# Kernel tuning notes

Hardware: AMD Instinct MI355X
Metric: run time of the kernel (lower is better)

## Reference

```python
import jax, jax.numpy as jnp
import numpy as np

N = 50000   # total nodes in batched graph
E = 400000  # directed edges
G = 512     # number of graphs in batch
F = 128     # input node feature dim
K = 4       # attention heads
H = 64      # hidden feats per head (flatten width = K*H = 256)
EPS = 1e-5  # BatchNorm eps


def _edge_softmax(e, dst, n):
    # softmax of per-edge scores over incoming edges of each dst node; e: [E, K]
    m = jax.ops.segment_max(e, dst, num_segments=n)
    ee = jnp.exp(e - m[dst])
    s = jax.ops.segment_sum(ee, dst, num_segments=n)
    return ee / s[dst]


def _gat_layer(x, W, al, ar, b, resW, src, dst, agg):
    # dgl GATConv with residual=True, LeakyReLU(0.2), bias, ReLU activation
    n = x.shape[0]
    z = (x @ W).reshape(n, K, H)                      # [N, K, H]
    el = jnp.einsum('nkh,kh->nk', z, al)              # [N, K]
    er = jnp.einsum('nkh,kh->nk', z, ar)
    e = jax.nn.leaky_relu(el[src] + er[dst], negative_slope=0.2)  # [E, K]
    a = _edge_softmax(e, dst, n)                      # [E, K]
    rst = jax.ops.segment_sum(a[:, :, None] * z[src], dst, num_segments=n)  # [N, K, H]
    res = (x @ resW).reshape(n, K, H) if resW is not None else x.reshape(n, K, H)
    rst = jax.nn.relu(rst + res + b.reshape(1, K, H))
    return rst.reshape(n, K * H) if agg == 'flatten' else rst.mean(axis=1)


def setup_inputs() -> dict:
    key = jax.random.key(0)
    ks = jax.random.split(key, 16)
    f32 = jnp.float32

    def p(k, shape):
        return jax.random.normal(k, shape, f32) * 0.1

    h = jax.random.normal(ks[0], (N, F), f32)
    src = jax.random.randint(ks[1], (E,), 0, N)
    dst = jax.random.randint(ks[2], (E,), 0, N)
    graph_ids = (jnp.arange(N) * G) // N  # sorted node->graph assignment, all segments nonempty

    return dict(
        h=h, src=src, dst=dst, graph_ids=graph_ids,
        W0=p(ks[3], (F, K * H)), al0=p(ks[4], (K, H)), ar0=p(ks[5], (K, H)),
        b0=jnp.zeros((K * H,), f32), resW0=p(ks[6], (F, K * H)),
        W1=p(ks[7], (K * H, K * H)), al1=p(ks[8], (K, H)), ar1=p(ks[9], (K, H)),
        b1=jnp.zeros((K * H,), f32),
        W2=p(ks[10], (K * H, K * H)), al2=p(ks[11], (K, H)), ar2=p(ks[12], (K, H)),
        b2=jnp.zeros((K * H,), f32),
        Wg=p(ks[13], (H, 1)), bg=jnp.zeros((1,), f32),
        Wm1=p(ks[14], (2 * H, H)), bm1=jnp.zeros((H,), f32),
        bn_g=jnp.ones((H,), f32), bn_b=jnp.zeros((H,), f32),
        bn_m=jnp.zeros((H,), f32), bn_v=jnp.ones((H,), f32),
        Wm2=p(ks[15], (H, 1)), bm2=jnp.zeros((1,), f32),
    )


def reference(h, src, dst, graph_ids, W0, al0, ar0, b0, resW0, W1, al1, ar1, b1,
              W2, al2, ar2, b2, Wg, bg, Wm1, bm1, bn_g, bn_b, bn_m, bn_v, Wm2, bm2):
    # 3 GAT layers: flatten, flatten, mean (dgllife GATPredictor default agg modes)
    x = _gat_layer(h, W0, al0, ar0, b0, resW0, src, dst, 'flatten')   # [N, 256]
    x = _gat_layer(x, W1, al1, ar1, b1, None, src, dst, 'flatten')    # [N, 256] (identity residual)
    x = _gat_layer(x, W2, al2, ar2, b2, None, src, dst, 'mean')       # [N, 64]
    # WeightedSumAndMax readout
    w = jax.nn.sigmoid(x @ Wg + bg)                                   # [N, 1]
    gs = jax.ops.segment_sum(w * x, graph_ids, num_segments=G)        # [G, 64]
    gm = jax.ops.segment_max(x, graph_ids, num_segments=G)            # [G, 64]
    gf = jnp.concatenate([gs, gm], axis=1)                            # [G, 128]
    # MLPPredictor (eval mode: dropout off, BatchNorm uses running stats)
    y = jax.nn.relu(gf @ Wm1 + bm1)
    y = (y - bn_m) / jnp.sqrt(bn_v + EPS) * bn_g + bn_b
    out = jax.nn.sigmoid(y @ Wm2 + bm2)                               # [G, 1]
    return out
```

## Files before the change

kernel.cpp:

```cpp
#include <hip/hip_runtime.h>
#include <math.h>


typedef _Float16 f16;
typedef _Float16 f16x4 __attribute__((ext_vector_type(4)));
typedef _Float16 f16x8 __attribute__((ext_vector_type(8)));
typedef float f32x16 __attribute__((ext_vector_type(16)));

__device__ __forceinline__ double wred_sumd(double v) {
#pragma unroll
  for (int m = 32; m > 0; m >>= 1) v += __shfl_xor(v, m, 64);
  return v;
}
__device__ __forceinline__ float wred_sum(float v) {
#pragma unroll
  for (int m = 32; m > 0; m >>= 1) v += __shfl_xor(v, m, 64);
  return v;
}

__global__ void k_hist(const int* __restrict__ dst, int* __restrict__ deg, int e) {
  int i = blockIdx.x * 256 + threadIdx.x;
  if (i < e) atomicAdd(&deg[dst[i]], 1);
}

__global__ void k_scan1(const int* __restrict__ deg, int* __restrict__ rowptr,
                        int* __restrict__ bsum, int n) {
  __shared__ int sh[256];
  int t = threadIdx.x;
  int base = blockIdx.x * 1024 + t * 4;
  int v0 = 0, v1 = 0, v2 = 0, v3 = 0;
  if (base + 0 < n) v0 = deg[base + 0];
  if (base + 1 < n) v1 = deg[base + 1];
  if (base + 2 < n) v2 = deg[base + 2];
  if (base + 3 < n) v3 = deg[base + 3];
  sh[t] = v0 + v1 + v2 + v3;
  __syncthreads();
  for (int off = 1; off < 256; off <<= 1) {
    int x = (t >= off) ? sh[t - off] : 0;
    __syncthreads();
    sh[t] += x;
    __syncthreads();
  }
  int excl = (t > 0) ? sh[t - 1] : 0;
  if (base + 0 < n) rowptr[base + 0] = excl;
  if (base + 1 < n) rowptr[base + 1] = excl + v0;
  if (base + 2 < n) rowptr[base + 2] = excl + v0 + v1;
  if (base + 3 < n) rowptr[base + 3] = excl + v0 + v1 + v2;
  if (t == 255) bsum[blockIdx.x] = sh[255];
}

__global__ void k_scan2(int* bsum, int nb) {
  if (threadIdx.x == 0 && blockIdx.x == 0) {
    int run = 0;
    for (int i = 0; i < nb; i++) { int v = bsum[i]; bsum[i] = run; run += v; }
  }
}

__global__ void k_scan3(int* __restrict__ rowptr, const int* __restrict__ bsum,
                        int n, int e) {
  int i = blockIdx.x * 256 + threadIdx.x;
  if (i < n) rowptr[i] += bsum[i >> 10];
  if (i == 0) rowptr[n] = e;
}

__global__ void k_scatter(const int* __restrict__ src, const int* __restrict__ dst,
                          const int* __restrict__ rowptr, int* __restrict__ cursor,
                          int* __restrict__ colsrc, int e) {
  int i = blockIdx.x * 256 + threadIdx.x;
  if (i < e) {
    int d = dst[i];
    int pos = rowptr[d] + atomicAdd(&cursor[d], 1);
    colsrc[pos] = src[i];
  }
}

__global__ __launch_bounds__(256) void k_split(const float* __restrict__ X,
                                               f16* __restrict__ X0,
                                               f16* __restrict__ X1, int n4) {
  int i = blockIdx.x * 256 + threadIdx.x;
  if (i >= n4) return;
  float4 v = *(const float4*)(X + (size_t)i * 4);
  f16x4 hi, lo;
  hi.x = (f16)v.x; lo.x = (f16)(v.x - (float)hi.x);
  hi.y = (f16)v.y; lo.y = (f16)(v.y - (float)hi.y);
  hi.z = (f16)v.z; lo.z = (f16)(v.z - (float)hi.z);
  hi.w = (f16)v.w; lo.w = (f16)(v.w - (float)hi.w);
  *(f16x4*)(X0 + (size_t)i * 4) = hi;
  *(f16x4*)(X1 + (size_t)i * 4) = lo;
}

__global__ void k_splitWT(const float* __restrict__ W, f16* __restrict__ P0,
                          f16* __restrict__ P1, int kin) {
  int c = blockIdx.x;
  for (int k = threadIdx.x; k < kin; k += blockDim.x) {
    float v = W[(size_t)k * 256 + c];
    f16 h0 = (f16)v;
    size_t off = ((size_t)(k >> 4) * 256 + c) * 16 + ((k >> 3) & 1) * 8 + (k & 7);
    P0[off] = h0;
    P1[off] = (f16)(v - (float)h0);
  }
}

template <int KIN>
__global__ __launch_bounds__(256) void k_gemm_mfma(
    const f16* __restrict__ X0, const f16* __restrict__ X1,
    const f16* __restrict__ WT0, const f16* __restrict__ WT1,
    float* __restrict__ C, int M) {
  __shared__ f16 aLDS[2][2][2][64][8];
  const int t = threadIdx.x;
  const int w = t >> 6;
  const int lane = t & 63;
  const int lo = lane & 31, g = lane >> 5;
  const int row0 = blockIdx.x * 64;

  f32x16 acc00, acc01, acc10, acc11;
#pragma unroll
  for (int i = 0; i < 16; i++) {
    acc00[i] = 0.f; acc01[i] = 0.f; acc10[i] = 0.f; acc11[i] = 0.f;
  }

  const size_t fb0 = (size_t)(w * 64 + lo) * 16 + g * 8;
  const size_t fb1 = (size_t)(w * 64 + 32 + lo) * 16 + g * 8;

  for (int k0 = 0; k0 < KIN; k0 += 32) {
    if (k0) __syncthreads();
#pragma unroll
    for (int ii = 0; ii < 2; ii++) {
      int c = t + ii * 256;
      int s = c >> 8, r = (c >> 2) & 63, hh = c & 3;
      int kh = hh >> 1, gg = hh & 1;
      int gr = row0 + r;
      if (gr > M - 1) gr = M - 1;
      const f16* Xs = s ? X1 : X0;
      *(float4*)&aLDS[s][r >> 5][kh][(gg << 5) | (r & 31)][0] =
          *(const float4*)&Xs[(size_t)gr * KIN + k0 + kh * 16 + gg * 8];
    }
    __syncthreads();
#pragma unroll
    for (int kh = 0; kh < 2; kh++) {
      const size_t base = (size_t)((k0 >> 4) + kh) * 4096;
      f16x8 a0r0 = *(const f16x8*)&aLDS[0][0][kh][lane][0];
      f16x8 a0r1 = *(const f16x8*)&aLDS[0][1][kh][lane][0];
      f16x8 a1r0 = *(const f16x8*)&aLDS[1][0][kh][lane][0];
      f16x8 a1r1 = *(const f16x8*)&aLDS[1][1][kh][lane][0];
      f16x8 b0c0 = *(const f16x8*)&WT0[base + fb0];
      f16x8 b0c1 = *(const f16x8*)&WT0[base + fb1];
      f16x8 b1c0 = *(const f16x8*)&WT1[base + fb0];
      f16x8 b1c1 = *(const f16x8*)&WT1[base + fb1];
      acc00 = __builtin_amdgcn_mfma_f32_32x32x16_f16(a0r0, b0c0, acc00, 0, 0, 0);
      acc01 = __builtin_amdgcn_mfma_f32_32x32x16_f16(a0r0, b0c1, acc01, 0, 0, 0);
      acc10 = __builtin_amdgcn_mfma_f32_32x32x16_f16(a0r1, b0c0, acc10, 0, 0, 0);
      acc11 = __builtin_amdgcn_mfma_f32_32x32x16_f16(a0r1, b0c1, acc11, 0, 0, 0);
      acc00 = __builtin_amdgcn_mfma_f32_32x32x16_f16(a0r0, b1c0, acc00, 0, 0, 0);
      acc01 = __builtin_amdgcn_mfma_f32_32x32x16_f16(a0r0, b1c1, acc01, 0, 0, 0);
      acc10 = __builtin_amdgcn_mfma_f32_32x32x16_f16(a0r1, b1c0, acc10, 0, 0, 0);
      acc11 = __builtin_amdgcn_mfma_f32_32x32x16_f16(a0r1, b1c1, acc11, 0, 0, 0);
      acc00 = __builtin_amdgcn_mfma_f32_32x32x16_f16(a1r0, b0c0, acc00, 0, 0, 0);
      acc01 = __builtin_amdgcn_mfma_f32_32x32x16_f16(a1r0, b0c1, acc01, 0, 0, 0);
      acc10 = __builtin_amdgcn_mfma_f32_32x32x16_f16(a1r1, b0c0, acc10, 0, 0, 0);
      acc11 = __builtin_amdgcn_mfma_f32_32x32x16_f16(a1r1, b0c1, acc11, 0, 0, 0);
    }
  }
  const int c0 = w * 64 + lo, c1 = w * 64 + 32 + lo;
#pragma unroll
  for (int reg = 0; reg < 16; reg++) {
    int rr = (reg & 3) + 8 * (reg >> 2) + 4 * g;
    int r0 = row0 + rr, r1 = row0 + 32 + rr;
    if (r0 < M) {
      C[(size_t)r0 * 256 + c0] = acc00[reg];
      C[(size_t)r0 * 256 + c1] = acc01[reg];
    }
    if (r1 < M) {
      C[(size_t)r1 * 256 + c0] = acc10[reg];
      C[(size_t)r1 * 256 + c1] = acc11[reg];
    }
  }
}

__global__ __launch_bounds__(256) void k_elr(const float* __restrict__ z,
                                             const float* __restrict__ al,
                                             const float* __restrict__ ar,
                                             float* __restrict__ el,
                                             float* __restrict__ er, int n) {
  int node = blockIdx.x * 4 + (threadIdx.x >> 6);
  int lane = threadIdx.x & 63;
  if (node >= n) return;
  const float* zr = z + (size_t)node * 256;
#pragma unroll
  for (int k = 0; k < 4; k++) {
    float zv = zr[k * 64 + lane];
    float pl = wred_sum(zv * al[k * 64 + lane]);
    float pr = wred_sum(zv * ar[k * 64 + lane]);
    if (lane == 0) {
      el[node * 4 + k] = pl;
      er[node * 4 + k] = pr;
    }
  }
}

__global__ __launch_bounds__(256) void k_att(const float* __restrict__ el,
                                             const float* __restrict__ er,
                                             const int* __restrict__ rowptr,
                                             const int* __restrict__ colsrc,
                                             float* __restrict__ a, int n) {
  int node = blockIdx.x * 4 + (threadIdx.x >> 6);
  int lane = threadIdx.x & 63;
  if (node >= n) return;
  int k = lane & 3, ii = lane >> 2;
  int base = rowptr[node];
  int deg = rowptr[node + 1] - base;
  if (deg == 0) return;
  float ernk = er[node * 4 + k];

  float m = -INFINITY;
  for (int i0 = 0; i0 < deg; i0 += 16) {
    int i = i0 + ii;
    if (i < deg) {
      int s = colsrc[base + i];
      float sc = el[s * 4 + k] + ernk;
      sc = (sc > 0.f) ? sc : 0.2f * sc;
      m = fmaxf(m, sc);
    }
  }
#pragma unroll
  for (int msk = 4; msk < 64; msk <<= 1) m = fmaxf(m, __shfl_xor(m, msk, 64));

  float ssum = 0.f;
  for (int i0 = 0; i0 < deg; i0 += 16) {
    int i = i0 + ii;
    if (i < deg) {
      int s = colsrc[base + i];
      float sc = el[s * 4 + k] + ernk;
      sc = (sc > 0.f) ? sc : 0.2f * sc;
      ssum += expf(sc - m);
    }
  }
#pragma unroll
  for (int msk = 4; msk < 64; msk <<= 1) ssum += __shfl_xor(ssum, msk, 64);
  float inv = 1.f / ssum;

  for (int i0 = 0; i0 < deg; i0 += 16) {
    int i = i0 + ii;
    if (i < deg) {
      int s = colsrc[base + i];
      float sc = el[s * 4 + k] + ernk;
      sc = (sc > 0.f) ? sc : 0.2f * sc;
      a[(size_t)(base + i) * 4 + k] = expf(sc - m) * inv;
    }
  }
}

template <int MEAN, int RESF16>
__global__ __launch_bounds__(256) void k_gather(
    const float* __restrict__ z, const float* __restrict__ a,
    const float* __restrict__ resf, const f16* __restrict__ R0,
    const f16* __restrict__ R1, const float* __restrict__ bias,
    const int* __restrict__ rowptr, const int* __restrict__ colsrc,
    float* __restrict__ out, f16* __restrict__ O0, f16* __restrict__ O1,
    float* __restrict__ wn, const float* __restrict__ Wg,
    const float* __restrict__ bg, int n) {
  const int t = threadIdx.x;
  const int w = t >> 6, lane = t & 63;
  int node = blockIdx.x * 4 + w;
  if (node > n - 1) node = n - 1;
  const int base = rowptr[node];
  const int deg = rowptr[node + 1] - base;
  const int k = lane >> 4;
  const char* zb = (const char*)z + lane * 16;

  float4 acc0 = {0, 0, 0, 0}, acc1 = {0, 0, 0, 0};
  float4 acc2 = {0, 0, 0, 0}, acc3 = {0, 0, 0, 0};
  int i = 0;
  for (; i + 4 <= deg; i += 4) {
    int s0 = colsrc[base + i + 0];
    int s1 = colsrc[base + i + 1];
    int s2 = colsrc[base + i + 2];
    int s3 = colsrc[base + i + 3];
    float a0 = a[(size_t)(base + i + 0) * 4 + k];
    float a1 = a[(size_t)(base + i + 1) * 4 + k];
    float a2 = a[(size_t)(base + i + 2) * 4 + k];
    float a3 = a[(size_t)(base + i + 3) * 4 + k];
    float4 z0 = *(const float4*)(zb + ((size_t)s0 << 10));
    float4 z1 = *(const float4*)(zb + ((size_t)s1 << 10));
    float4 z2 = *(const float4*)(zb + ((size_t)s2 << 10));
    float4 z3 = *(const float4*)(zb + ((size_t)s3 << 10));
    acc0.x = fmaf(a0, z0.x, acc0.x); acc0.y = fmaf(a0, z0.y, acc0.y);
    acc0.z = fmaf(a0, z0.z, acc0.z); acc0.w = fmaf(a0, z0.w, acc0.w);
    acc1.x = fmaf(a1, z1.x, acc1.x); acc1.y = fmaf(a1, z1.y, acc1.y);
    acc1.z = fmaf(a1, z1.z, acc1.z); acc1.w = fmaf(a1, z1.w, acc1.w);
    acc2.x = fmaf(a2, z2.x, acc2.x); acc2.y = fmaf(a2, z2.y, acc2.y);
    acc2.z = fmaf(a2, z2.z, acc2.z); acc2.w = fmaf(a2, z2.w, acc2.w);
    acc3.x = fmaf(a3, z3.x, acc3.x); acc3.y = fmaf(a3, z3.y, acc3.y);
    acc3.z = fmaf(a3, z3.z, acc3.z); acc3.w = fmaf(a3, z3.w, acc3.w);
  }
  for (; i < deg; i++) {
    int s = colsrc[base + i];
    float av = a[(size_t)(base + i) * 4 + k];
    float4 zv = *(const float4*)(zb + ((size_t)s << 10));
    acc0.x = fmaf(av, zv.x, acc0.x); acc0.y = fmaf(av, zv.y, acc0.y);
    acc0.z = fmaf(av, zv.z, acc0.z); acc0.w = fmaf(av, zv.w, acc0.w);
  }

  size_t o = (size_t)node * 256 + lane * 4;
  float4 rv;
  if (RESF16) {
    f16x4 rh = *(const f16x4*)(R0 + o);
    f16x4 rl = *(const f16x4*)(R1 + o);
    rv.x = (float)rh.x + (float)rl.x;
    rv.y = (float)rh.y + (float)rl.y;
    rv.z = (float)rh.z + (float)rl.z;
    rv.w = (float)rh.w + (float)rl.w;
  } else {
    rv = *(const float4*)(resf + o);
  }
  float4 bv = *(const float4*)(bias + lane * 4);
  float4 v;
  v.x = fmaxf(((acc0.x + acc1.x) + (acc2.x + acc3.x)) + rv.x + bv.x, 0.f);
  v.y = fmaxf(((acc0.y + acc1.y) + (acc2.y + acc3.y)) + rv.y + bv.y, 0.f);
  v.z = fmaxf(((acc0.z + acc1.z) + (acc2.z + acc3.z)) + rv.z + bv.z, 0.f);
  v.w = fmaxf(((acc0.w + acc1.w) + (acc2.w + acc3.w)) + rv.w + bv.w, 0.f);

  if (!MEAN) {
    f16x4 hi, lo;
    hi.x = (f16)v.x; lo.x = (f16)(v.x - (float)hi.x);
    hi.y = (f16)v.y; lo.y = (f16)(v.y - (float)hi.y);
    hi.z = (f16)v.z; lo.z = (f16)(v.z - (float)hi.z);
    hi.w = (f16)v.w; lo.w = (f16)(v.w - (float)hi.w);
    *(f16x4*)(O0 + o) = hi;
    *(f16x4*)(O1 + o) = lo;
  } else {
    __shared__ float tmp[4][256];
    *(float4*)&tmp[w][lane * 4] = v;
    __syncthreads();
    float xv = 0.25f * (tmp[w][lane] + tmp[w][lane + 64] + tmp[w][lane + 128] +
                        tmp[w][lane + 192]);
    out[(size_t)node * 64 + lane] = xv;
    double s = wred_sumd((double)xv * (double)Wg[lane]);
    if (lane == 0)
      wn[node] = (float)(1.0 / (1.0 + exp(-(s + (double)bg[0]))));
  }
}

__global__ __launch_bounds__(64) void k_readout(const float* __restrict__ x2,
                                                const float* __restrict__ wn,
                                                float* __restrict__ gf, int n,
                                                int g) {
  int gi = blockIdx.x;
  int lane = threadIdx.x;
  long long start = ((long long)gi * n + g - 1) / g;
  long long end = ((long long)(gi + 1) * n + g - 1) / g;
  double s = 0.0;
  float mx = -INFINITY;
  for (long long nd = start; nd < end; nd++) {
    float xv = x2[nd * 64 + lane];
    s += (double)wn[nd] * (double)xv;
    mx = fmaxf(mx, xv);
  }
  gf[gi * 128 + lane] = (float)s;
  gf[gi * 128 + 64 + lane] = mx;
}

__global__ __launch_bounds__(64) void k_mlp(const float* __restrict__ gf,
                                            const float* __restrict__ Wm1,
                                            const float* __restrict__ bm1,
                                            const float* __restrict__ bng,
                                            const float* __restrict__ bnb,
                                            const float* __restrict__ bnm,
                                            const float* __restrict__ bnv,
                                            const float* __restrict__ Wm2,
                                            const float* __restrict__ bm2,
                                            float* __restrict__ out) {
  int gi = blockIdx.x;
  int h = threadIdx.x;
  double y = (double)bm1[h];
  for (int i = 0; i < 128; i++)
    y += (double)gf[gi * 128 + i] * (double)Wm1[i * 64 + h];
  y = (y > 0.0) ? y : 0.0;
  y = (y - (double)bnm[h]) / sqrt((double)bnv[h] + 1e-5) * (double)bng[h] +
      (double)bnb[h];
  double v = wred_sumd(y * (double)Wm2[h]);
  if (h == 0) {
    double s = v + (double)bm2[0];
    out[gi] = (float)(1.0 / (1.0 + exp(-s)));
  }
}

extern "C" void kernel_launch(void* const* d_in, const int* in_sizes, int n_in,
                              void* d_out, int out_size, void* d_ws,
                              size_t ws_size, hipStream_t stream) {
  const float* h    = (const float*)d_in[0];
  const int*   src  = (const int*)d_in[1];
  const int*   dst  = (const int*)d_in[2];
  const float* W0    = (const float*)d_in[4];
  const float* al0   = (const float*)d_in[5];
  const float* ar0   = (const float*)d_in[6];
  const float* b0    = (const float*)d_in[7];
  const float* resW0 = (const float*)d_in[8];
  const float* W1    = (const float*)d_in[9];
  const float* al1   = (const float*)d_in[10];
  const float* ar1   = (const float*)d_in[11];
  const float* b1    = (const float*)d_in[12];
  const float* W2    = (const float*)d_in[13];
  const float* al2   = (const float*)d_in[14];
  const float* ar2   = (const float*)d_in[15];
  const float* b2    = (const float*)d_in[16];
  const float* Wg    = (const float*)d_in[17];
  const float* bg    = (const float*)d_in[18];
  const float* Wm1   = (const float*)d_in[19];
  const float* bm1   = (const float*)d_in[20];
  const float* bng   = (const float*)d_in[21];
  const float* bnb   = (const float*)d_in[22];
  const float* bnm   = (const float*)d_in[23];
  const float* bnv   = (const float*)d_in[24];
  const float* Wm2   = (const float*)d_in[25];
  const float* bm2   = (const float*)d_in[26];

  const int n = in_sizes[0] / 128;
  const int e = in_sizes[1];
  const int g = out_size;

  char* ws = (char*)d_ws;
  size_t off = 0;
  auto alloc = [&](size_t bytes) {
    void* p = ws + off;
    off += (bytes + 255) & ~(size_t)255;
    return p;
  };
  int*   deg    = (int*)alloc((size_t)n * 4);
  int*   cursor = (int*)alloc((size_t)n * 4);
  int*   rowptr = (int*)alloc((size_t)(n + 1) * 4);
  int*   bsum   = (int*)alloc(256 * 4);
  int*   colsrc = (int*)alloc((size_t)e * 4);
  float* el     = (float*)alloc((size_t)n * 4 * 4);
  float* er     = (float*)alloc((size_t)n * 4 * 4);
  float* abuf   = (float*)alloc((size_t)e * 4 * 4);
  float* bufA   = (float*)alloc((size_t)n * 256 * 4);
  float* bufB   = (float*)alloc((size_t)n * 256 * 4);
  float* x2     = (float*)alloc((size_t)n * 64 * 4);
  float* wn     = (float*)alloc((size_t)n * 4);
  float* gf     = (float*)alloc((size_t)g * 128 * 4);
  f16*   sA0    = (f16*)alloc((size_t)n * 256 * 2);
  f16*   sA1    = (f16*)alloc((size_t)n * 256 * 2);
  f16*   sB0    = (f16*)alloc((size_t)n * 256 * 2);
  f16*   sB1    = (f16*)alloc((size_t)n * 256 * 2);
  f16*   wtA0   = (f16*)alloc(65536 * 2);
  f16*   wtA1   = (f16*)alloc(65536 * 2);
  f16*   wtR0   = (f16*)alloc(65536 * 2);
  f16*   wtR1   = (f16*)alloc(65536 * 2);
  f16*   wtB0   = (f16*)alloc(65536 * 2);
  f16*   wtB1   = (f16*)alloc(65536 * 2);
  f16*   wtC0   = (f16*)alloc(65536 * 2);
  f16*   wtC1   = (f16*)alloc(65536 * 2);
  (void)ws_size;
  (void)n_in;

  hipMemsetAsync(deg, 0, (size_t)n * 4, stream);
  hipMemsetAsync(cursor, 0, (size_t)n * 4, stream);

  const int eb = (e + 255) / 256;
  const int nb = (n + 1023) / 1024;
  k_hist<<<eb, 256, 0, stream>>>(dst, deg, e);
  k_scan1<<<nb, 256, 0, stream>>>(deg, rowptr, bsum, n);
  k_scan2<<<1, 64, 0, stream>>>(bsum, nb);
  k_scan3<<<(n + 255) / 256, 256, 0, stream>>>(rowptr, bsum, n, e);
  k_scatter<<<eb, 256, 0, stream>>>(src, dst, rowptr, cursor, colsrc, e);

  k_splitWT<<<256, 256, 0, stream>>>(W0, wtA0, wtA1, 128);
  k_splitWT<<<256, 256, 0, stream>>>(resW0, wtR0, wtR1, 128);
  k_splitWT<<<256, 256, 0, stream>>>(W1, wtB0, wtB1, 256);
  k_splitWT<<<256, 256, 0, stream>>>(W2, wtC0, wtC1, 256);

  const int mb64 = (n + 63) / 64;
  const int n4 = (n + 3) / 4;
  const int sp128 = (n * 128 / 4 + 255) / 256;

  k_split<<<sp128, 256, 0, stream>>>(h, sA0, sA1, n * 128 / 4);
  k_gemm_mfma<128><<<mb64, 256, 0, stream>>>(sA0, sA1, wtA0, wtA1, bufA, n);
  k_gemm_mfma<128><<<mb64, 256, 0, stream>>>(sA0, sA1, wtR0, wtR1, bufB, n);
  k_elr<<<n4, 256, 0, stream>>>(bufA, al0, ar0, el, er, n);
  k_att<<<n4, 256, 0, stream>>>(el, er, rowptr, colsrc, abuf, n);
  k_gather<0, 0><<<n4, 256, 0, stream>>>(bufA, abuf, bufB, nullptr, nullptr,
                                         b0, rowptr, colsrc, nullptr, sB0, sB1,
                                         nullptr, nullptr, nullptr, n);

  k_gemm_mfma<256><<<mb64, 256, 0, stream>>>(sB0, sB1, wtB0, wtB1, bufA, n);
  k_elr<<<n4, 256, 0, stream>>>(bufA, al1, ar1, el, er, n);
  k_att<<<n4, 256, 0, stream>>>(el, er, rowptr, colsrc, abuf, n);
  k_gather<0, 1><<<n4, 256, 0, stream>>>(bufA, abuf, nullptr, sB0, sB1, b1,
                                         rowptr, colsrc, nullptr, sA0, sA1,
                                         nullptr, nullptr, nullptr, n);

  k_gemm_mfma<256><<<mb64, 256, 0, stream>>>(sA0, sA1, wtC0, wtC1, bufA, n);
  k_elr<<<n4, 256, 0, stream>>>(bufA, al2, ar2, el, er, n);
  k_att<<<n4, 256, 0, stream>>>(el, er, rowptr, colsrc, abuf, n);
  k_gather<1, 1><<<n4, 256, 0, stream>>>(bufA, abuf, nullptr, sA0, sA1, b2,
                                         rowptr, colsrc, x2, nullptr, nullptr,
                                         wn, Wg, bg, n);

  k_readout<<<g, 64, 0, stream>>>(x2, wn, gf, n, g);
  k_mlp<<<g, 64, 0, stream>>>(gf, Wm1, bm1, bng, bnb, bnm, bnv, Wm2, bm2,
                              (float*)d_out);
}
```

Before: 579.1 us.

## Fuse edge softmax into gather kernel and halve GEMM row tile

The separate attention kernel is removed. Each gather wavefront now computes the per-head max and sum over its incoming edges and recomputes the attention weights inline while accumulating neighbour features, so the E×4 attention buffer is never written or read. The MFMA GEMM tile also shrinks from 64 to 32 rows per block, doubling the block count for more parallelism, though each B-fragment load now feeds fewer MFMAs. The trade-off is extra el gathers and exp evaluations per edge inside the gather, plus more global weight traffic per output row.

```diff
diff --git a/kernel.cpp b/kernel.cpp
--- a/kernel.cpp
+++ b/kernel.cpp
@@ -106,73 +106,57 @@
     const f16* __restrict__ X0, const f16* __restrict__ X1,
     const f16* __restrict__ WT0, const f16* __restrict__ WT1,
     float* __restrict__ C, int M) {
-  __shared__ f16 aLDS[2][2][2][64][8];
+  __shared__ f16 aLDS[2][2][64][8];
   const int t = threadIdx.x;
   const int w = t >> 6;
   const int lane = t & 63;
   const int lo = lane & 31, g = lane >> 5;
-  const int row0 = blockIdx.x * 64;
-
-  f32x16 acc00, acc01, acc10, acc11;
-#pragma unroll
-  for (int i = 0; i < 16; i++) {
-    acc00[i] = 0.f; acc01[i] = 0.f; acc10[i] = 0.f; acc11[i] = 0.f;
-  }
+  const int row0 = blockIdx.x * 32;
+
+  f32x16 acc0, acc1;
+#pragma unroll
+  for (int i = 0; i < 16; i++) { acc0[i] = 0.f; acc1[i] = 0.f; }
 
   const size_t fb0 = (size_t)(w * 64 + lo) * 16 + g * 8;
   const size_t fb1 = (size_t)(w * 64 + 32 + lo) * 16 + g * 8;
 
   for (int k0 = 0; k0 < KIN; k0 += 32) {
     if (k0) __syncthreads();
-#pragma unroll
-    for (int ii = 0; ii < 2; ii++) {
-      int c = t + ii * 256;
-      int s = c >> 8, r = (c >> 2) & 63, hh = c & 3;
+    {
+      int s = t >> 7, r = (t >> 2) & 31, hh = t & 3;
       int kh = hh >> 1, gg = hh & 1;
       int gr = row0 + r;
       if (gr > M - 1) gr = M - 1;
       const f16* Xs = s ? X1 : X0;
-      *(float4*)&aLDS[s][r >> 5][kh][(gg << 5) | (r & 31)][0] =
+      *(float4*)&aLDS[s][kh][(gg << 5) | r][0] =
           *(const float4*)&Xs[(size_t)gr * KIN + k0 + kh * 16 + gg * 8];
     }
     __syncthreads();
 #pragma unroll
     for (int kh = 0; kh < 2; kh++) {
-      const size_t base = (size_t)((k0 >> 4) + kh) * 4096;
-      f16x8 a0r0 = *(const f16x8*)&aLDS[0][0][kh][lane][0];
-      f16x8 a0r1 = *(const f16x8*)&aLDS[0][1][kh][lane][0];
-      f16x8 a1r0 = *(const f16x8*)&aLDS[1][0][kh][lane][0];
-      f16x8 a1r1 = *(const f16x8*)&aLDS[1][1][kh][lane][0];
-      f16x8 b0c0 = *(const f16x8*)&WT0[base + fb0];
-      f16x8 b0c1 = *(const f16x8*)&WT0[base + fb1];
-      f16x8 b1c0 = *(const f16x8*)&WT1[base + fb0];
-      f16x8 b1c1 = *(const f16x8*)&WT1[base + fb1];
-      acc00 = __builtin_amdgcn_mfma_f32_32x32x16_f16(a0r0, b0c0, acc00, 0, 0, 0);
-      acc01 = __builtin_amdgcn_mfma_f32_32x32x16_f16(a0r0, b0c1, acc01, 0, 0, 0);
-      acc10 = __builtin_amdgcn_mfma_f32_32x32x16_f16(a0r1, b0c0, acc10, 0, 0, 0);
-      acc11 = __builtin_amdgcn_mfma_f32_32x32x16_f16(a0r1, b0c1, acc11, 0, 0, 0);
-      acc00 = __builtin_amdgcn_mfma_f32_32x32x16_f16(a0r0, b1c0, acc00, 0, 0, 0);
-      acc01 = __builtin_amdgcn_mfma_f32_32x32x16_f16(a0r0, b1c1, acc01, 0, 0, 0);
-      acc10 = __builtin_amdgcn_mfma_f32_32x32x16_f16(a0r1, b1c0, acc10, 0, 0, 0);
-      acc11 = __builtin_amdgcn_mfma_f32_32x32x16_f16(a0r1, b1c1, acc11, 0, 0, 0);
-      acc00 = __builtin_amdgcn_mfma_f32_32x32x16_f16(a1r0, b0c0, acc00, 0, 0, 0);
-      acc01 = __builtin_amdgcn_mfma_f32_32x32x16_f16(a1r0, b0c1, acc01, 0, 0, 0);
-      acc10 = __builtin_amdgcn_mfma_f32_32x32x16_f16(a1r1, b0c0, acc10, 0, 0, 0);
-      acc11 = __builtin_amdgcn_mfma_f32_32x32x16_f16(a1r1, b0c1, acc11, 0, 0, 0);
+      const size_t bbase = (size_t)((k0 >> 4) + kh) * 4096;
+      f16x8 a0 = *(const f16x8*)&aLDS[0][kh][lane][0];
+      f16x8 a1 = *(const f16x8*)&aLDS[1][kh][lane][0];
+      f16x8 b0c0 = *(const f16x8*)&WT0[bbase + fb0];
+      f16x8 b0c1 = *(const f16x8*)&WT0[bbase + fb1];
+      f16x8 b1c0 = *(const f16x8*)&WT1[bbase + fb0];
+      f16x8 b1c1 = *(const f16x8*)&WT1[bbase + fb1];
+      acc0 = __builtin_amdgcn_mfma_f32_32x32x16_f16(a0, b0c0, acc0, 0, 0, 0);
+      acc1 = __builtin_amdgcn_mfma_f32_32x32x16_f16(a0, b0c1, acc1, 0, 0, 0);
+      acc0 = __builtin_amdgcn_mfma_f32_32x32x16_f16(a0, b1c0, acc0, 0, 0, 0);
+      acc1 = __builtin_amdgcn_mfma_f32_32x32x16_f16(a0, b1c1, acc1, 0, 0, 0);
+      acc0 = __builtin_amdgcn_mfma_f32_32x32x16_f16(a1, b0c0, acc0, 0, 0, 0);
+      acc1 = __builtin_amdgcn_mfma_f32_32x32x16_f16(a1, b0c1, acc1, 0, 0, 0);
     }
   }
   const int c0 = w * 64 + lo, c1 = w * 64 + 32 + lo;
 #pragma unroll
   for (int reg = 0; reg < 16; reg++) {
     int rr = (reg & 3) + 8 * (reg >> 2) + 4 * g;
-    int r0 = row0 + rr, r1 = row0 + 32 + rr;
+    int r0 = row0 + rr;
     if (r0 < M) {
-      C[(size_t)r0 * 256 + c0] = acc00[reg];
-      C[(size_t)r0 * 256 + c1] = acc01[reg];
-    }
-    if (r1 < M) {
-      C[(size_t)r1 * 256 + c0] = acc10[reg];
-      C[(size_t)r1 * 256 + c1] = acc11[reg];
+      C[(size_t)r0 * 256 + c0] = acc0[reg];
+      C[(size_t)r0 * 256 + c1] = acc1[reg];
     }
   }
 }
@@ -198,76 +182,52 @@
   }
 }
 
-__global__ __launch_bounds__(256) void k_att(const float* __restrict__ el,
-                                             const float* __restrict__ er,
-                                             const int* __restrict__ rowptr,
-                                             const int* __restrict__ colsrc,
-                                             float* __restrict__ a, int n) {
-  int node = blockIdx.x * 4 + (threadIdx.x >> 6);
-  int lane = threadIdx.x & 63;
-  if (node >= n) return;
-  int k = lane & 3, ii = lane >> 2;
-  int base = rowptr[node];
-  int deg = rowptr[node + 1] - base;
-  if (deg == 0) return;
-  float ernk = er[node * 4 + k];
-
-  float m = -INFINITY;
-  for (int i0 = 0; i0 < deg; i0 += 16) {
-    int i = i0 + ii;
-    if (i < deg) {
-      int s = colsrc[base + i];
-      float sc = el[s * 4 + k] + ernk;
-      sc = (sc > 0.f) ? sc : 0.2f * sc;
-      m = fmaxf(m, sc);
-    }
-  }
-#pragma unroll
-  for (int msk = 4; msk < 64; msk <<= 1) m = fmaxf(m, __shfl_xor(m, msk, 64));
-
-  float ssum = 0.f;
-  for (int i0 = 0; i0 < deg; i0 += 16) {
-    int i = i0 + ii;
-    if (i < deg) {
-      int s = colsrc[base + i];
-      float sc = el[s * 4 + k] + ernk;
-      sc = (sc > 0.f) ? sc : 0.2f * sc;
-      ssum += expf(sc - m);
-    }
-  }
-#pragma unroll
-  for (int msk = 4; msk < 64; msk <<= 1) ssum += __shfl_xor(ssum, msk, 64);
-  float inv = 1.f / ssum;
-
-  for (int i0 = 0; i0 < deg; i0 += 16) {
-    int i = i0 + ii;
-    if (i < deg) {
-      int s = colsrc[base + i];
-      float sc = el[s * 4 + k] + ernk;
-      sc = (sc > 0.f) ? sc : 0.2f * sc;
-      a[(size_t)(base + i) * 4 + k] = expf(sc - m) * inv;
-    }
-  }
-}
-
 template <int MEAN, int RESF16>
 __global__ __launch_bounds__(256) void k_gather(
-    const float* __restrict__ z, const float* __restrict__ a,
-    const float* __restrict__ resf, const f16* __restrict__ R0,
-    const f16* __restrict__ R1, const float* __restrict__ bias,
-    const int* __restrict__ rowptr, const int* __restrict__ colsrc,
-    float* __restrict__ out, f16* __restrict__ O0, f16* __restrict__ O1,
-    float* __restrict__ wn, const float* __restrict__ Wg,
-    const float* __restrict__ bg, int n) {
+    const float* __restrict__ z, const float* __restrict__ el,
+    const float* __restrict__ er, const float* __restrict__ resf,
+    const f16* __restrict__ R0, const f16* __restrict__ R1,
+    const float* __restrict__ bias, const int* __restrict__ rowptr,
+    const int* __restrict__ colsrc, float* __restrict__ out,
+    f16* __restrict__ O0, f16* __restrict__ O1, float* __restrict__ wn,
+    const float* __restrict__ Wg, const float* __restrict__ bg, int n) {
   const int t = threadIdx.x;
   const int w = t >> 6, lane = t & 63;
   int node = blockIdx.x * 4 + w;
   if (node > n - 1) node = n - 1;
   const int base = rowptr[node];
   const int deg = rowptr[node + 1] - base;
-  const int k = lane >> 4;
+  const int k = lane >> 4, j = lane & 15;
+  const float ernk = er[node * 4 + k];
+
+  float m = -INFINITY;
+  for (int i0 = 0; i0 < deg; i0 += 16) {
+    int i = i0 + j;
+    if (i < deg) {
+      int s = colsrc[base + i];
+      float sc = el[s * 4 + k] + ernk;
+      sc = (sc > 0.f) ? sc : 0.2f * sc;
+      m = fmaxf(m, sc);
+    }
+  }
+#pragma unroll
+  for (int msk = 1; msk < 16; msk <<= 1) m = fmaxf(m, __shfl_xor(m, msk, 64));
+
+  float ssum = 0.f;
+  for (int i0 = 0; i0 < deg; i0 += 16) {
+    int i = i0 + j;
+    if (i < deg) {
+      int s = colsrc[base + i];
+      float sc = el[s * 4 + k] + ernk;
+      sc = (sc > 0.f) ? sc : 0.2f * sc;
+      ssum += expf(sc - m);
+    }
+  }
+#pragma unroll
+  for (int msk = 1; msk < 16; msk <<= 1) ssum += __shfl_xor(ssum, msk, 64);
+  const float inv = 1.f / ssum;
+
   const char* zb = (const char*)z + lane * 16;
-
   float4 acc0 = {0, 0, 0, 0}, acc1 = {0, 0, 0, 0};
   float4 acc2 = {0, 0, 0, 0}, acc3 = {0, 0, 0, 0};
   int i = 0;
@@ -276,14 +236,18 @@
     int s1 = colsrc[base + i + 1];
     int s2 = colsrc[base + i + 2];
     int s3 = colsrc[base + i + 3];
-    float a0 = a[(size_t)(base + i + 0) * 4 + k];
-    float a1 = a[(size_t)(base + i + 1) * 4 + k];
-    float a2 = a[(size_t)(base + i + 2) * 4 + k];
-    float a3 = a[(size_t)(base + i + 3) * 4 + k];
     float4 z0 = *(const float4*)(zb + ((size_t)s0 << 10));
     float4 z1 = *(const float4*)(zb + ((size_t)s1 << 10));
     float4 z2 = *(const float4*)(zb + ((size_t)s2 << 10));
     float4 z3 = *(const float4*)(zb + ((size_t)s3 << 10));
+    float c0 = el[s0 * 4 + k] + ernk; c0 = (c0 > 0.f) ? c0 : 0.2f * c0;
+    float c1 = el[s1 * 4 + k] + ernk; c1 = (c1 > 0.f) ? c1 : 0.2f * c1;
+    float c2 = el[s2 * 4 + k] + ernk; c2 = (c2 > 0.f) ? c2 : 0.2f * c2;
+    float c3 = el[s3 * 4 + k] + ernk; c3 = (c3 > 0.f) ? c3 : 0.2f * c3;
+    float a0 = expf(c0 - m) * inv;
+    float a1 = expf(c1 - m) * inv;
+    float a2 = expf(c2 - m) * inv;
+    float a3 = expf(c3 - m) * inv;
     acc0.x = fmaf(a0, z0.x, acc0.x); acc0.y = fmaf(a0, z0.y, acc0.y);
     acc0.z = fmaf(a0, z0.z, acc0.z); acc0.w = fmaf(a0, z0.w, acc0.w);
     acc1.x = fmaf(a1, z1.x, acc1.x); acc1.y = fmaf(a1, z1.y, acc1.y);
@@ -295,8 +259,9 @@
   }
   for (; i < deg; i++) {
     int s = colsrc[base + i];
-    float av = a[(size_t)(base + i) * 4 + k];
     float4 zv = *(const float4*)(zb + ((size_t)s << 10));
+    float c = el[s * 4 + k] + ernk; c = (c > 0.f) ? c : 0.2f * c;
+    float av = expf(c - m) * inv;
     acc0.x = fmaf(av, zv.x, acc0.x); acc0.y = fmaf(av, zv.y, acc0.y);
     acc0.z = fmaf(av, zv.z, acc0.z); acc0.w = fmaf(av, zv.w, acc0.w);
   }
@@ -433,7 +398,6 @@
   int*   colsrc = (int*)alloc((size_t)e * 4);
   float* el     = (float*)alloc((size_t)n * 4 * 4);
   float* er     = (float*)alloc((size_t)n * 4 * 4);
-  float* abuf   = (float*)alloc((size_t)e * 4 * 4);
   float* bufA   = (float*)alloc((size_t)n * 256 * 4);
   float* bufB   = (float*)alloc((size_t)n * 256 * 4);
   float* x2     = (float*)alloc((size_t)n * 64 * 4);
@@ -470,30 +434,27 @@
   k_splitWT<<<256, 256, 0, stream>>>(W1, wtB0, wtB1, 256);
   k_splitWT<<<256, 256, 0, stream>>>(W2, wtC0, wtC1, 256);
 
-  const int mb64 = (n + 63) / 64;
+  const int mb32 = (n + 31) / 32;
   const int n4 = (n + 3) / 4;
   const int sp128 = (n * 128 / 4 + 255) / 256;
 
   k_split<<<sp128, 256, 0, stream>>>(h, sA0, sA1, n * 128 / 4);
-  k_gemm_mfma<128><<<mb64, 256, 0, stream>>>(sA0, sA1, wtA0, wtA1, bufA, n);
-  k_gemm_mfma<128><<<mb64, 256, 0, stream>>>(sA0, sA1, wtR0, wtR1, bufB, n);
+  k_gemm_mfma<128><<<mb32, 256, 0, stream>>>(sA0, sA1, wtA0, wtA1, bufA, n);
+  k_gemm_mfma<128><<<mb32, 256, 0, stream>>>(sA0, sA1, wtR0, wtR1, bufB, n);
   k_elr<<<n4, 256, 0, stream>>>(bufA, al0, ar0, el, er, n);
-  k_att<<<n4, 256, 0, stream>>>(el, er, rowptr, colsrc, abuf, n);
-  k_gather<0, 0><<<n4, 256, 0, stream>>>(bufA, abuf, bufB, nullptr, nullptr,
+  k_gather<0, 0><<<n4, 256, 0, stream>>>(bufA, el, er, bufB, nullptr, nullptr,
                                          b0, rowptr, colsrc, nullptr, sB0, sB1,
                                          nullptr, nullptr, nullptr, n);
 
-  k_gemm_mfma<256><<<mb64, 256, 0, stream>>>(sB0, sB1, wtB0, wtB1, bufA, n);
+  k_gemm_mfma<256><<<mb32, 256, 0, stream>>>(sB0, sB1, wtB0, wtB1, bufA, n);
   k_elr<<<n4, 256, 0, stream>>>(bufA, al1, ar1, el, er, n);
-  k_att<<<n4, 256, 0, stream>>>(el, er, rowptr, colsrc, abuf, n);
-  k_gather<0, 1><<<n4, 256, 0, stream>>>(bufA, abuf, nullptr, sB0, sB1, b1,
+  k_gather<0, 1><<<n4, 256, 0, stream>>>(bufA, el, er, nullptr, sB0, sB1, b1,
                                          rowptr, colsrc, nullptr, sA0, sA1,
                                          nullptr, nullptr, nullptr, n);
 
-  k_gemm_mfma<256><<<mb64, 256, 0, stream>>>(sA0, sA1, wtC0, wtC1, bufA, n);
+  k_gemm_mfma<256><<<mb32, 256, 0, stream>>>(sA0, sA1, wtC0, wtC1, bufA, n);
   k_elr<<<n4, 256, 0, stream>>>(bufA, al2, ar2, el, er, n);
-  k_att<<<n4, 256, 0, stream>>>(el, er, rowptr, colsrc, abuf, n);
-  k_gather<1, 1><<<n4, 256, 0, stream>>>(bufA, abuf, nullptr, sA0, sA1, b2,
+  k_gather<1, 1><<<n4, 256, 0, stream>>>(bufA, el, er, nullptr, sA0, sA1, b2,
                                          rowptr, colsrc, x2, nullptr, nullptr,
                                          wn, Wg, bg, n);
 
```

New measurement: 515.0 us. 1.12x faster.
